# Kernel tuning notes

Measured on AMD Instinct MI355X. Metric: run time of the kernel, lower is better.

The kernel has to match this reference:

```python
import jax, jax.numpy as jnp
import numpy as np

B, N, E, H = 4, 512, 512, 8
HD = E // H // 2            # 32; per-head value dim is 2*HD = 64
C_IN = 64                   # u_proj Conv2d in_channels
LAMBDA_INIT = 0.8 - 0.6 * float(np.exp(-0.3 * (28.0 / 28.0) * (1 - 1)))  # layer_idx=1, depth=28 -> 0.2
LN_EPS = 1e-5


def setup_inputs() -> dict:
    key = jax.random.key(0)
    ks = jax.random.split(key, 13)
    x = jax.random.normal(ks[0], (B, N, E), dtype=jnp.float32)
    u = jax.random.normal(ks[1], (B, N, N, C_IN), dtype=jnp.float32)
    umask = jax.random.randint(ks[2], (B, N, N, 2 * H), 0, 2).astype(bool)
    s = 0.02
    v_w = jax.random.normal(ks[3], (E, E), dtype=jnp.float32) * s        # nn.Linear weight [out,in]
    out_w = jax.random.normal(ks[4], (E, E), dtype=jnp.float32) * s
    uproj_w = jax.random.normal(ks[5], (2 * H, C_IN), dtype=jnp.float32) * s  # 1x1 conv kernel
    uproj_b = jax.random.normal(ks[6], (2 * H,), dtype=jnp.float32) * s
    lq1 = jax.random.normal(ks[7], (E,), dtype=jnp.float32) * 0.1
    lk1 = jax.random.normal(ks[8], (E,), dtype=jnp.float32) * 0.1
    lq2 = jax.random.normal(ks[9], (E,), dtype=jnp.float32) * 0.1
    lk2 = jax.random.normal(ks[10], (E,), dtype=jnp.float32) * 0.1
    ln_w = jnp.ones((2 * HD,), dtype=jnp.float32)
    ln_b = jnp.zeros((2 * HD,), dtype=jnp.float32)
    return {"x": x, "u": u, "umask": umask, "v_w": v_w, "out_w": out_w,
            "uproj_w": uproj_w, "uproj_b": uproj_b,
            "lq1": lq1, "lk1": lk1, "lq2": lq2, "lk2": lk2,
            "ln_w": ln_w, "ln_b": ln_b}


def reference(x, u, umask, v_w, out_w, uproj_w, uproj_b, lq1, lk1, lq2, lk2, ln_w, ln_b):
    b, n, e = x.shape
    # v projection -> [B, H, N, 2*HD]
    v = jnp.einsum('bne,fe->bnf', x, v_w).reshape(b, n, H, 2 * HD).transpose(0, 2, 1, 3)
    # 1x1 conv on u: [B,N,N,C_IN] -> [B,N,N,2H]
    ue = jnp.einsum('bnmc,hc->bnmh', u, uproj_w) + uproj_b
    ue = jnp.where(umask, -jnp.inf, ue)
    # transpose(3,1): [B,N,N,2H] -> [B,2H,N,N]; softmax over last (key) axis
    aw = jax.nn.softmax(jnp.transpose(ue, (0, 3, 2, 1)), axis=-1)
    lam1 = jnp.exp(jnp.sum(lq1 * lk1))
    lam2 = jnp.exp(jnp.sum(lq2 * lk2))
    lam = lam1 - lam2 + LAMBDA_INIT
    aw = aw.reshape(b, H, 2, n, n)
    diff = aw[:, :, 0] - lam * aw[:, :, 1]          # [B,H,N,N]
    attn = jnp.einsum('bhnm,bhmd->bhnd', diff, v)   # [B,H,N,2HD]
    # sub-LayerNorm over last dim
    mu = jnp.mean(attn, axis=-1, keepdims=True)
    var = jnp.mean(jnp.square(attn - mu), axis=-1, keepdims=True)
    attn = (attn - mu) * jax.lax.rsqrt(var + LN_EPS) * ln_w + ln_b
    attn = attn.transpose(0, 2, 1, 3).reshape(b, n, e)
    return jnp.einsum('bne,fe->bnf', attn, out_w)
```

## Files before the change

kernel.cpp:

```cpp
#include <hip/hip_runtime.h>
#include <math.h>

typedef _Float16 f16x8 __attribute__((ext_vector_type(8)));
typedef _Float16 f16x4 __attribute__((ext_vector_type(4)));
typedef float    f32x4 __attribute__((ext_vector_type(4)));

constexpr int kB  = 4;
constexpr int kN  = 512;
constexpr int kE  = 512;
constexpr int kH  = 8;
constexpr int kH2 = 16;
constexpr int kC  = 64;
constexpr int kDV = 64;
constexpr float kLamInit = 0.2f;

__global__ __launch_bounds__(256) void prep_kernel(
    const float* __restrict__ x, const float* __restrict__ vw,
    const float* __restrict__ ow,
    const float* __restrict__ lq1, const float* __restrict__ lk1,
    const float* __restrict__ lq2, const float* __restrict__ lk2,
    _Float16* __restrict__ x16, _Float16* __restrict__ w16v,
    _Float16* __restrict__ w16o, float* __restrict__ lam_out) {
  const int bid = blockIdx.x;
  if (bid < 1536) {
    const float* src; _Float16* dst; int base;
    if (bid < 1024)      { src = x;  dst = x16;  base = bid; }
    else if (bid < 1280) { src = vw; dst = w16v; base = bid - 1024; }
    else                 { src = ow; dst = w16o; base = bid - 1280; }
    const int i = base * 256 + threadIdx.x;
    const float4 v = ((const float4*)src)[i];
    union { _Float16 h[4]; uint2 u2; } P;
    P.h[0]=(_Float16)v.x; P.h[1]=(_Float16)v.y;
    P.h[2]=(_Float16)v.z; P.h[3]=(_Float16)v.w;
    *(uint2*)(dst + i * 4) = P.u2;
  } else if (threadIdx.x < 64) {
    float s1 = 0.f, s2 = 0.f;
    for (int i = threadIdx.x; i < kE; i += 64) { s1 += lq1[i]*lk1[i]; s2 += lq2[i]*lk2[i]; }
    #pragma unroll
    for (int o = 32; o; o >>= 1) { s1 += __shfl_xor(s1, o); s2 += __shfl_xor(s2, o); }
    if (threadIdx.x == 0) lam_out[0] = expf(s1) - expf(s2) + kLamInit;
  }
}

__global__ __launch_bounds__(256) void hgemm16f(const _Float16* __restrict__ A16,
                                                const _Float16* __restrict__ W16,
                                                float* __restrict__ C,
                                                int M, int F, int K) {
  const int tid = threadIdx.x, lane = tid & 63, wv = tid >> 6;
  const int l15 = lane & 15, l4 = lane >> 4;
  const int m0 = blockIdx.y * 64 + wv * 16;
  const int f0 = blockIdx.x * 64;
  f32x4 acc[4] = {{0,0,0,0},{0,0,0,0},{0,0,0,0},{0,0,0,0}};
  const _Float16* Ap = A16 + (size_t)(m0 + l15) * K + l4 * 8;
  const _Float16* Wp = W16 + (size_t)(f0 + l15) * K + l4 * 8;
  for (int k0 = 0; k0 < K; k0 += 32) {
    const f16x8 af = *(const f16x8*)(Ap + k0);
    #pragma unroll
    for (int t = 0; t < 4; ++t) {
      const f16x8 bf = *(const f16x8*)(Wp + (size_t)t * 16 * K + k0);
      acc[t] = __builtin_amdgcn_mfma_f32_16x16x32_f16(af, bf, acc[t], 0, 0, 0);
    }
  }
  #pragma unroll
  for (int t = 0; t < 4; ++t)
    #pragma unroll
    for (int r = 0; r < 4; ++r)
      C[(size_t)(m0 + l4 * 4 + r) * F + f0 + t * 16 + l15] = acc[t][r];
}

__global__ __launch_bounds__(256) void hgemmT_v(const _Float16* __restrict__ W16,
                                                const _Float16* __restrict__ X16,
                                                _Float16* __restrict__ Vt) {
  const int tid = threadIdx.x, lane = tid & 63, wv = tid >> 6;
  const int l15 = lane & 15, l4 = lane >> 4;
  const int f0 = blockIdx.y * 64 + wv * 16;
  const int n0 = blockIdx.x * 64;
  f32x4 acc[4] = {{0,0,0,0},{0,0,0,0},{0,0,0,0},{0,0,0,0}};
  const _Float16* Ap = W16 + (size_t)(f0 + l15) * kE + l4 * 8;
  const _Float16* Bp = X16 + (size_t)(n0 + l15) * kE + l4 * 8;
  for (int k0 = 0; k0 < kE; k0 += 32) {
    const f16x8 af = *(const f16x8*)(Ap + k0);
    #pragma unroll
    for (int t = 0; t < 4; ++t) {
      const f16x8 bf = *(const f16x8*)(Bp + (size_t)t * 16 * kE + k0);
      acc[t] = __builtin_amdgcn_mfma_f32_16x16x32_f16(af, bf, acc[t], 0, 0, 0);
    }
  }
  #pragma unroll
  for (int t = 0; t < 4; ++t)
    #pragma unroll
    for (int r = 0; r < 4; ++r) {
      const int f  = f0 + l4 * 4 + r;
      const int ng = n0 + t * 16 + l15;
      const int bb = ng >> 9, n = ng & 511;
      Vt[(((size_t)((bb * kH + (f >> 6)) * kDV) + (f & 63)) * kN) + n] = (_Float16)acc[t][r];
    }
}

__global__ __launch_bounds__(512, 4) void fused_attn4(
    const float* __restrict__ u, const int* __restrict__ umask,
    const float* __restrict__ uw, const float* __restrict__ ub,
    const _Float16* __restrict__ Vt,
    _Float16* __restrict__ Opart, float* __restrict__ Spart) {
  __shared__ _Float16 P[16 * 648];
  __shared__ float S_lds[8][16][17];
  const int tid = threadIdx.x, lane = tid & 63, wv = tid >> 6;
  const int l15 = lane & 15, l4 = lane >> 4;
  const int qt = blockIdx.x, kh = blockIdx.y, b = blockIdx.z;
  const int q0 = qt * 16;
  const int kstart = kh * 128;

  f16x8 bfrag[2];
  #pragma unroll
  for (int ch = 0; ch < 2; ++ch) {
    const float* wp = uw + l15 * 64 + ch * 32 + l4 * 8;
    const float4 wa = *(const float4*)wp;
    const float4 wb = *(const float4*)(wp + 4);
    f16x8 bf;
    bf[0]=(_Float16)wa.x; bf[1]=(_Float16)wa.y; bf[2]=(_Float16)wa.z; bf[3]=(_Float16)wa.w;
    bf[4]=(_Float16)wb.x; bf[5]=(_Float16)wb.y; bf[6]=(_Float16)wb.z; bf[7]=(_Float16)wb.w;
    bfrag[ch] = bf;
  }
  const float bias = ub[l15];

  float s_acc[4] = {};
  f32x4 oacc[2][4];
  #pragma unroll
  for (int s = 0; s < 2; ++s)
    #pragma unroll
    for (int d = 0; d < 4; ++d) oacc[s][d] = (f32x4){0,0,0,0};

  for (int t = 0; t < 4; ++t) {
    const int k0 = kstart + t * 32;
    _Float16 vals[4][4];
    #pragma unroll
    for (int kk = 0; kk < 4; ++kk) {
      const int k = k0 + wv * 4 + kk;
      const float* up = u + (((size_t)(b * kN + k)) * kN + q0 + l15) * kC + l4 * 8;
      f32x4 acc = {0.f, 0.f, 0.f, 0.f};
      #pragma unroll
      for (int ch = 0; ch < 2; ++ch) {
        const float4 a0 = *(const float4*)(up + ch * 32);
        const float4 a1 = *(const float4*)(up + ch * 32 + 4);
        f16x8 af;
        af[0]=(_Float16)a0.x; af[1]=(_Float16)a0.y; af[2]=(_Float16)a0.z; af[3]=(_Float16)a0.w;
        af[4]=(_Float16)a1.x; af[5]=(_Float16)a1.y; af[6]=(_Float16)a1.z; af[7]=(_Float16)a1.w;
        acc = __builtin_amdgcn_mfma_f32_16x16x32_f16(af, bfrag[ch], acc, 0, 0, 0);
      }
      const int* mrow = umask + (((size_t)(b * kN + k)) * kN + q0) * kH2 + l15;
      #pragma unroll
      for (int r = 0; r < 4; ++r) {
        const float e = mrow[(l4 * 4 + r) * kH2] ? 0.f : __expf(acc[r] + bias);
        s_acc[r] += e;
        vals[r][kk] = (_Float16)e;
      }
    }
    #pragma unroll
    for (int r = 0; r < 4; ++r) {
      union { _Float16 h[4]; uint2 u2; } PK;
      #pragma unroll
      for (int kk = 0; kk < 4; ++kk) PK.h[kk] = vals[r][kk];
      *(uint2*)&P[l15 * 648 + (l4 * 4 + r) * 40 + wv * 4] = PK.u2;
    }
    __syncthreads();
    f16x8 va[4];
    #pragma unroll
    for (int dt = 0; dt < 4; ++dt)
      va[dt] = *(const f16x8*)(Vt + (((size_t)((b * kH + wv) * kDV + dt * 16 + l15)) * kN) + k0 + l4 * 8);
    #pragma unroll
    for (int s = 0; s < 2; ++s) {
      const f16x8 pb = *(const f16x8*)&P[(wv * 2 + s) * 648 + l15 * 40 + l4 * 8];
      #pragma unroll
      for (int dt = 0; dt < 4; ++dt)
        oacc[s][dt] = __builtin_amdgcn_mfma_f32_16x16x32_f16(va[dt], pb, oacc[s][dt], 0, 0, 0);
    }
    __syncthreads();
  }

  #pragma unroll
  for (int r = 0; r < 4; ++r) S_lds[wv][l15][l4 * 4 + r] = s_acc[r];
  __syncthreads();
  const int blk = (b * 4 + kh) * 32 + qt;
  if (tid < 256) {
    const int h2 = tid >> 4, q = tid & 15;
    float S = 0.f;
    #pragma unroll
    for (int j = 0; j < 8; ++j) S += S_lds[j][h2][q];
    Spart[(size_t)blk * 256 + h2 * 16 + q] = S;
  }
  _Float16* ob = Opart + (size_t)blk * 16384;
  #pragma unroll
  for (int s = 0; s < 2; ++s)
    #pragma unroll
    for (int dt = 0; dt < 4; ++dt)
      #pragma unroll
      for (int r = 0; r < 4; ++r)
        ob[((size_t)(s * 8 + wv) * 64 + dt * 16 + l4 * 4 + r) * 16 + l15] =
            (_Float16)oacc[s][dt][r];
}

__global__ __launch_bounds__(256) void combine3(
    const _Float16* __restrict__ Opart, const float* __restrict__ Spart,
    const float* __restrict__ lam_p, const float* __restrict__ ln_w,
    const float* __restrict__ ln_b, _Float16* __restrict__ a16) {
  __shared__ float vsh[64][17];
  __shared__ float inv_sh[2][16];
  const int tid = threadIdx.x;
  const int qt = blockIdx.x, h = blockIdx.y, b = blockIdx.z;
  if (tid < 32) {
    const int s = tid >> 4, q = tid & 15;
    float S = 0.f;
    #pragma unroll
    for (int kh = 0; kh < 4; ++kh)
      S += Spart[(size_t)((b * 4 + kh) * 32 + qt) * 256 + (h * 2 + s) * 16 + q];
    inv_sh[s][q] = (s ? lam_p[0] : 1.0f) / S;
  }
  float a0[4] = {}, a1[4] = {};
  #pragma unroll
  for (int kh = 0; kh < 4; ++kh) {
    const size_t base = (size_t)((b * 4 + kh) * 32 + qt) * 16384;
    const f16x4 p0 = *(const f16x4*)(Opart + base + (size_t)(0 * 8 + h) * 1024 + tid * 4);
    const f16x4 p1 = *(const f16x4*)(Opart + base + (size_t)(1 * 8 + h) * 1024 + tid * 4);
    #pragma unroll
    for (int j = 0; j < 4; ++j) { a0[j] += (float)p0[j]; a1[j] += (float)p1[j]; }
  }
  __syncthreads();
  {
    const int d = tid >> 2, q0i = (tid & 3) * 4;
    #pragma unroll
    for (int j = 0; j < 4; ++j)
      vsh[d][q0i + j] = a0[j] * inv_sh[0][q0i + j] - a1[j] * inv_sh[1][q0i + j];
  }
  __syncthreads();
  const int q = tid >> 4, i = tid & 15;
  float vv[4], s1 = 0.f, s2 = 0.f;
  #pragma unroll
  for (int jj = 0; jj < 4; ++jj) {
    vv[jj] = vsh[i * 4 + jj][q];
    s1 += vv[jj]; s2 += vv[jj] * vv[jj];
  }
  #pragma unroll
  for (int o = 1; o < 16; o <<= 1) { s1 += __shfl_xor(s1, o); s2 += __shfl_xor(s2, o); }
  const float mu = s1 * (1.0f / kDV);
  const float var = s2 * (1.0f / kDV) - mu * mu;
  const float rstd = rsqrtf(var + 1e-5f);
  union { _Float16 hh[4]; uint2 u2; } PK;
  #pragma unroll
  for (int jj = 0; jj < 4; ++jj)
    PK.hh[jj] = (_Float16)((vv[jj] - mu) * rstd * ln_w[i * 4 + jj] + ln_b[i * 4 + jj]);
  *(uint2*)(a16 + ((size_t)(b * kN + qt * 16 + q)) * kE + h * kDV + i * 4) = PK.u2;
}

extern "C" void kernel_launch(void* const* d_in, const int* in_sizes, int n_in,
                              void* d_out, int out_size, void* d_ws, size_t ws_size,
                              hipStream_t stream) {
  const float* x     = (const float*)d_in[0];
  const float* u     = (const float*)d_in[1];
  const int*   umask = (const int*)d_in[2];
  const float* v_w   = (const float*)d_in[3];
  const float* out_w = (const float*)d_in[4];
  const float* uw    = (const float*)d_in[5];
  const float* ubias = (const float*)d_in[6];
  const float* lq1   = (const float*)d_in[7];
  const float* lk1   = (const float*)d_in[8];
  const float* lq2   = (const float*)d_in[9];
  const float* lk2   = (const float*)d_in[10];
  const float* ln_w  = (const float*)d_in[11];
  const float* ln_b  = (const float*)d_in[12];
  float* out = (float*)d_out;

  char* ws = (char*)d_ws;
  const size_t sz_half = (size_t)kB * kN * kE * 2;
  const size_t sz_w16  = (size_t)kE * kE * 2;
  const size_t sz_op   = (size_t)512 * 16384 * 2;
  const size_t sz_sp   = (size_t)512 * 256 * 4;
  const size_t off_x16 = 256;
  const size_t off_wv  = off_x16 + sz_half;
  const size_t off_wo  = off_wv + sz_w16;
  const size_t off_vt  = off_wo + sz_w16;
  const size_t off_a16 = off_vt + sz_half;
  const size_t off_op  = off_a16 + sz_half;
  const size_t off_sp  = off_op + sz_op;
  if (ws_size < off_sp + sz_sp) return;
  float*    lam   = (float*)(ws);
  _Float16* x16   = (_Float16*)(ws + off_x16);
  _Float16* w16v  = (_Float16*)(ws + off_wv);
  _Float16* w16o  = (_Float16*)(ws + off_wo);
  _Float16* Vt    = (_Float16*)(ws + off_vt);
  _Float16* a16   = (_Float16*)(ws + off_a16);
  _Float16* Opart = (_Float16*)(ws + off_op);
  float*    Spart = (float*)(ws + off_sp);

  prep_kernel<<<dim3(1537), dim3(256), 0, stream>>>(
      x, v_w, out_w, lq1, lk1, lq2, lk2, x16, w16v, w16o, lam);
  hgemmT_v<<<dim3(32, 8), dim3(256), 0, stream>>>(w16v, x16, Vt);
  fused_attn4<<<dim3(kN / 16, 4, kB), dim3(512), 0, stream>>>(
      u, umask, uw, ubias, Vt, Opart, Spart);
  combine3<<<dim3(kN / 16, kH, kB), dim3(256), 0, stream>>>(
      Opart, Spart, lam, ln_w, ln_b, a16);
  hgemm16f<<<dim3(kE / 64, (kB * kN) / 64), dim3(256), 0, stream>>>(
      a16, w16o, out, kB * kN, kE, kE);
}
```

Before: 119.8 us.

## Fuse split-K combine and LayerNorm into output projection GEMM

Merges the combine/LayerNorm kernel with the output-projection GEMM. Each block loops over all 8 heads to build a 16-row normalized activation tile in LDS, then runs the MFMA GEMM against half of the output weight columns. This drops one kernel launch and the fp16 activation buffer round-trip through global memory. In exchange, each (b, query-tile) combine is done twice, once per output half, and the grid shrinks to 256 blocks with a serial head loop.

```diff
diff --git a/kernel.cpp b/kernel.cpp
--- a/kernel.cpp
+++ b/kernel.cpp
@@ -42,32 +42,6 @@
   }
 }
 
-__global__ __launch_bounds__(256) void hgemm16f(const _Float16* __restrict__ A16,
-                                                const _Float16* __restrict__ W16,
-                                                float* __restrict__ C,
-                                                int M, int F, int K) {
-  const int tid = threadIdx.x, lane = tid & 63, wv = tid >> 6;
-  const int l15 = lane & 15, l4 = lane >> 4;
-  const int m0 = blockIdx.y * 64 + wv * 16;
-  const int f0 = blockIdx.x * 64;
-  f32x4 acc[4] = {{0,0,0,0},{0,0,0,0},{0,0,0,0},{0,0,0,0}};
-  const _Float16* Ap = A16 + (size_t)(m0 + l15) * K + l4 * 8;
-  const _Float16* Wp = W16 + (size_t)(f0 + l15) * K + l4 * 8;
-  for (int k0 = 0; k0 < K; k0 += 32) {
-    const f16x8 af = *(const f16x8*)(Ap + k0);
-    #pragma unroll
-    for (int t = 0; t < 4; ++t) {
-      const f16x8 bf = *(const f16x8*)(Wp + (size_t)t * 16 * K + k0);
-      acc[t] = __builtin_amdgcn_mfma_f32_16x16x32_f16(af, bf, acc[t], 0, 0, 0);
-    }
-  }
-  #pragma unroll
-  for (int t = 0; t < 4; ++t)
-    #pragma unroll
-    for (int r = 0; r < 4; ++r)
-      C[(size_t)(m0 + l4 * 4 + r) * F + f0 + t * 16 + l15] = acc[t][r];
-}
-
 __global__ __launch_bounds__(256) void hgemmT_v(const _Float16* __restrict__ W16,
                                                 const _Float16* __restrict__ X16,
                                                 _Float16* __restrict__ Vt) {
@@ -199,56 +173,81 @@
             (_Float16)oacc[s][dt][r];
 }
 
-__global__ __launch_bounds__(256) void combine3(
+__global__ __launch_bounds__(256) void combine_out(
     const _Float16* __restrict__ Opart, const float* __restrict__ Spart,
     const float* __restrict__ lam_p, const float* __restrict__ ln_w,
-    const float* __restrict__ ln_b, _Float16* __restrict__ a16) {
+    const float* __restrict__ ln_b, const _Float16* __restrict__ w16o,
+    float* __restrict__ out) {
+  __shared__ _Float16 a_lds[16][520];
   __shared__ float vsh[64][17];
   __shared__ float inv_sh[2][16];
   const int tid = threadIdx.x;
-  const int qt = blockIdx.x, h = blockIdx.y, b = blockIdx.z;
-  if (tid < 32) {
-    const int s = tid >> 4, q = tid & 15;
-    float S = 0.f;
-    #pragma unroll
-    for (int kh = 0; kh < 4; ++kh)
-      S += Spart[(size_t)((b * 4 + kh) * 32 + qt) * 256 + (h * 2 + s) * 16 + q];
-    inv_sh[s][q] = (s ? lam_p[0] : 1.0f) / S;
-  }
-  float a0[4] = {}, a1[4] = {};
-  #pragma unroll
-  for (int kh = 0; kh < 4; ++kh) {
-    const size_t base = (size_t)((b * 4 + kh) * 32 + qt) * 16384;
-    const f16x4 p0 = *(const f16x4*)(Opart + base + (size_t)(0 * 8 + h) * 1024 + tid * 4);
-    const f16x4 p1 = *(const f16x4*)(Opart + base + (size_t)(1 * 8 + h) * 1024 + tid * 4);
-    #pragma unroll
-    for (int j = 0; j < 4; ++j) { a0[j] += (float)p0[j]; a1[j] += (float)p1[j]; }
+  const int fh = blockIdx.x, qt = blockIdx.y, b = blockIdx.z;
+  const float lam = lam_p[0];
+
+  for (int h = 0; h < 8; ++h) {
+    if (tid < 32) {
+      const int s = tid >> 4, q = tid & 15;
+      float S = 0.f;
+      #pragma unroll
+      for (int kh = 0; kh < 4; ++kh)
+        S += Spart[(size_t)((b * 4 + kh) * 32 + qt) * 256 + (h * 2 + s) * 16 + q];
+      inv_sh[s][q] = (s ? lam : 1.0f) / S;
+    }
+    float a0[4] = {}, a1[4] = {};
+    #pragma unroll
+    for (int kh = 0; kh < 4; ++kh) {
+      const size_t base = (size_t)((b * 4 + kh) * 32 + qt) * 16384;
+      const f16x4 p0 = *(const f16x4*)(Opart + base + (size_t)(0 * 8 + h) * 1024 + tid * 4);
+      const f16x4 p1 = *(const f16x4*)(Opart + base + (size_t)(1 * 8 + h) * 1024 + tid * 4);
+      #pragma unroll
+      for (int j = 0; j < 4; ++j) { a0[j] += (float)p0[j]; a1[j] += (float)p1[j]; }
+    }
+    __syncthreads();
+    {
+      const int d = tid >> 2, q0i = (tid & 3) * 4;
+      #pragma unroll
+      for (int j = 0; j < 4; ++j)
+        vsh[d][q0i + j] = a0[j] * inv_sh[0][q0i + j] - a1[j] * inv_sh[1][q0i + j];
+    }
+    __syncthreads();
+    const int q = tid >> 4, i = tid & 15;
+    float vv[4], s1 = 0.f, s2 = 0.f;
+    #pragma unroll
+    for (int jj = 0; jj < 4; ++jj) {
+      vv[jj] = vsh[i * 4 + jj][q];
+      s1 += vv[jj]; s2 += vv[jj] * vv[jj];
+    }
+    #pragma unroll
+    for (int o = 1; o < 16; o <<= 1) { s1 += __shfl_xor(s1, o); s2 += __shfl_xor(s2, o); }
+    const float mu = s1 * (1.0f / kDV);
+    const float var = s2 * (1.0f / kDV) - mu * mu;
+    const float rstd = rsqrtf(var + 1e-5f);
+    #pragma unroll
+    for (int jj = 0; jj < 4; ++jj)
+      a_lds[q][h * kDV + i * 4 + jj] =
+          (_Float16)((vv[jj] - mu) * rstd * ln_w[i * 4 + jj] + ln_b[i * 4 + jj]);
   }
   __syncthreads();
-  {
-    const int d = tid >> 2, q0i = (tid & 3) * 4;
-    #pragma unroll
-    for (int j = 0; j < 4; ++j)
-      vsh[d][q0i + j] = a0[j] * inv_sh[0][q0i + j] - a1[j] * inv_sh[1][q0i + j];
-  }
-  __syncthreads();
-  const int q = tid >> 4, i = tid & 15;
-  float vv[4], s1 = 0.f, s2 = 0.f;
-  #pragma unroll
-  for (int jj = 0; jj < 4; ++jj) {
-    vv[jj] = vsh[i * 4 + jj][q];
-    s1 += vv[jj]; s2 += vv[jj] * vv[jj];
-  }
-  #pragma unroll
-  for (int o = 1; o < 16; o <<= 1) { s1 += __shfl_xor(s1, o); s2 += __shfl_xor(s2, o); }
-  const float mu = s1 * (1.0f / kDV);
-  const float var = s2 * (1.0f / kDV) - mu * mu;
-  const float rstd = rsqrtf(var + 1e-5f);
-  union { _Float16 hh[4]; uint2 u2; } PK;
-  #pragma unroll
-  for (int jj = 0; jj < 4; ++jj)
-    PK.hh[jj] = (_Float16)((vv[jj] - mu) * rstd * ln_w[i * 4 + jj] + ln_b[i * 4 + jj]);
-  *(uint2*)(a16 + ((size_t)(b * kN + qt * 16 + q)) * kE + h * kDV + i * 4) = PK.u2;
+
+  const int lane = tid & 63, wv = tid >> 6;
+  const int l15 = lane & 15, l4 = lane >> 4;
+  const int f0 = fh * 256 + wv * 64;
+  f32x4 acc[4] = {{0,0,0,0},{0,0,0,0},{0,0,0,0},{0,0,0,0}};
+  const _Float16* Wp = w16o + (size_t)(f0 + l15) * kE + l4 * 8;
+  for (int k0 = 0; k0 < kE; k0 += 32) {
+    const f16x8 af = *(const f16x8*)&a_lds[l15][k0 + l4 * 8];
+    #pragma unroll
+    for (int ft = 0; ft < 4; ++ft) {
+      const f16x8 bf = *(const f16x8*)(Wp + (size_t)ft * 16 * kE + k0);
+      acc[ft] = __builtin_amdgcn_mfma_f32_16x16x32_f16(af, bf, acc[ft], 0, 0, 0);
+    }
+  }
+  #pragma unroll
+  for (int ft = 0; ft < 4; ++ft)
+    #pragma unroll
+    for (int r = 0; r < 4; ++r)
+      out[(size_t)(b * kN + qt * 16 + l4 * 4 + r) * kE + f0 + ft * 16 + l15] = acc[ft][r];
 }
 
 extern "C" void kernel_launch(void* const* d_in, const int* in_sizes, int n_in,
@@ -278,8 +277,7 @@
   const size_t off_wv  = off_x16 + sz_half;
   const size_t off_wo  = off_wv + sz_w16;
   const size_t off_vt  = off_wo + sz_w16;
-  const size_t off_a16 = off_vt + sz_half;
-  const size_t off_op  = off_a16 + sz_half;
+  const size_t off_op  = off_vt + sz_half;
   const size_t off_sp  = off_op + sz_op;
   if (ws_size < off_sp + sz_sp) return;
   float*    lam   = (float*)(ws);
@@ -287,7 +285,6 @@
   _Float16* w16v  = (_Float16*)(ws + off_wv);
   _Float16* w16o  = (_Float16*)(ws + off_wo);
   _Float16* Vt    = (_Float16*)(ws + off_vt);
-  _Float16* a16   = (_Float16*)(ws + off_a16);
   _Float16* Opart = (_Float16*)(ws + off_op);
   float*    Spart = (float*)(ws + off_sp);
 
@@ -296,8 +293,6 @@
   hgemmT_v<<<dim3(32, 8), dim3(256), 0, stream>>>(w16v, x16, Vt);
   fused_attn4<<<dim3(kN / 16, 4, kB), dim3(512), 0, stream>>>(
       u, umask, uw, ubias, Vt, Opart, Spart);
-  combine3<<<dim3(kN / 16, kH, kB), dim3(256), 0, stream>>>(
-      Opart, Spart, lam, ln_w, ln_b, a16);
-  hgemm16f<<<dim3(kE / 64, (kB * kN) / 64), dim3(256), 0, stream>>>(
-      a16, w16o, out, kB * kN, kE, kE);
-}
+  combine_out<<<dim3(2, kN / 16, kB), dim3(256), 0, stream>>>(
+      Opart, Spart, lam, ln_w, ln_b, w16o, out);
+}
```

Result: no change. 118.0 us (-1.5%).
